# Performance work log

Measured on AMD Instinct MI355X. Metric: run time of the kernel, lower is better.

## Reference

```python
import jax, jax.numpy as jnp
import numpy as np

NC, NV, C, H, L = 60000, 256, 128, 4, 3
D = C // H
E1, E2 = 600000, 240000
VPG = 4  # virtual nodes per graph; batch = NV // VPG = 64


def setup_inputs() -> dict:
    key = jax.random.key(0)
    ks = iter(jax.random.split(key, 64))
    def rn(shape, scale=1.0):
        return jax.random.normal(next(ks), shape, dtype=jnp.float32) * scale
    sC = 1.0 / np.sqrt(C)
    sD = 1.0 / np.sqrt(D)
    return dict(
        x_cell=rn((NC, C)), x_vcell=rn((NV, C)),
        Wk=rn((L, 2, C, C), sC), bk=jnp.zeros((L, 2, C), jnp.float32),
        Wq=rn((L, 2, C, C), sC), bq=jnp.zeros((L, 2, C), jnp.float32),
        Wv=rn((L, 2, C, C), sC), bv=jnp.zeros((L, 2, C), jnp.float32),
        Wa=rn((L, 2, C, C), sC), ba=jnp.zeros((L, 2, C), jnp.float32),
        skip=jnp.ones((L, 2), jnp.float32),
        arel=rn((L, 2, H, D, D), sD), mrel=rn((L, 2, H, D, D), sD),
        prel=jnp.ones((L, 2, H), jnp.float32),
        Wk_o=rn((L, C, 1), sC), bk_o=jnp.zeros((L, 1), jnp.float32),
        Wq_o=rn((L, C, 1), sC), bq_o=jnp.zeros((L, 1), jnp.float32),
        Wv_o=rn((L, C, 1), sC), bv_o=jnp.zeros((L, 1), jnp.float32),
        Wa_o=rn((L, 1, 1)), ba_o=jnp.zeros((L, 1), jnp.float32),
        arel_o=jnp.ones((L, 1, 1, 1), jnp.float32),
        mrel_o=jnp.ones((L, 1, 1, 1), jnp.float32),
        prel_o=jnp.ones((L, 1), jnp.float32),
        fc_W=rn((VPG, 1), 0.5), fc_b=jnp.zeros((1,), jnp.float32),
        mlp_W1=rn((1, 2)), mlp_b1=jnp.zeros((2,), jnp.float32),
        mlp_W2=rn((2, 1), 0.7), mlp_b2=jnp.zeros((1,), jnp.float32),
        src_cc=jax.random.randint(next(ks), (E1,), 0, NC, dtype=jnp.int32),
        dst_cc=jax.random.randint(next(ks), (E1,), 0, NC, dtype=jnp.int32),
        src_cv=jax.random.randint(next(ks), (E2,), 0, NC, dtype=jnp.int32),
        dst_cv=jax.random.randint(next(ks), (E2,), 0, NV, dtype=jnp.int32),
    )


def _seg_softmax(logits, seg, n):
    # numerically stable softmax over edges grouped by destination node
    m = jax.ops.segment_max(logits, seg, num_segments=n)
    e = jnp.exp(logits - m[seg])
    s = jax.ops.segment_sum(e, seg, num_segments=n)
    return e / s[seg]


def _attn(k_src, q_dst, v_src, a_r, m_r, p_r, src, dst, n_dst, d):
    # HGT relation-specific attention: gather -> softmax per dst -> scatter
    krel = jnp.einsum('nhd,hde->nhe', k_src, a_r)
    vrel = jnp.einsum('nhd,hde->nhe', v_src, m_r)
    logits = (q_dst[dst] * krel[src]).sum(-1) * p_r / jnp.sqrt(jnp.float32(d))  # [E,H]
    alpha = _seg_softmax(logits, dst, n_dst)
    return jax.ops.segment_sum(alpha[..., None] * vrel[src], dst, num_segments=n_dst)


def _forward(x_cell, x_vcell, Wk, bk, Wq, bq, Wv, bv, Wa, ba, skip,
             arel, mrel, prel, Wk_o, bk_o, Wq_o, bq_o, Wv_o, bv_o, Wa_o, ba_o,
             arel_o, mrel_o, prel_o, fc_W, fc_b, mlp_W1, mlp_b1, mlp_W2, mlp_b2,
             src_cc, dst_cc, src_cv, dst_cv):
    nc, nv = x_cell.shape[0], x_vcell.shape[0]
    gelu = jax.nn.gelu
    xc, xv = x_cell, x_vcell
    outs = []
    for li in range(L):
        def lin(x, W, b):
            return (x @ W + b).reshape(x.shape[0], H, D)
        kc = lin(xc, Wk[li, 0], bk[li, 0])
        qc = lin(xc, Wq[li, 0], bq[li, 0])
        vc = lin(xc, Wv[li, 0], bv[li, 0])
        qv = lin(xv, Wq[li, 1], bq[li, 1])
        # in_conv: cell->cell and cell->vcell message passing
        agg_c = _attn(kc, qc, vc, arel[li, 0], mrel[li, 0], prel[li, 0], src_cc, dst_cc, nc, D)
        agg_v = _attn(kc, qv, vc, arel[li, 1], mrel[li, 1], prel[li, 1], src_cv, dst_cv, nv, D)
        oc = gelu(agg_c.reshape(nc, C)) @ Wa[li, 0] + ba[li, 0]
        ov = gelu(agg_v.reshape(nv, C)) @ Wa[li, 1] + ba[li, 1]
        bc = jax.nn.sigmoid(skip[li, 0])
        bvv = jax.nn.sigmoid(skip[li, 1])
        xc = bc * oc + (1.0 - bc) * xc
        xv = bvv * ov + (1.0 - bvv) * xv
        # out_conv (hid->1, 1 head) on virtual edges only
        ko = (xc @ Wk_o[li] + bk_o[li]).reshape(nc, 1, 1)
        qo = (xv @ Wq_o[li] + bq_o[li]).reshape(nv, 1, 1)
        vo = (xc @ Wv_o[li] + bv_o[li]).reshape(nc, 1, 1)
        aggo = _attn(ko, qo, vo, arel_o[li], mrel_o[li], prel_o[li], src_cv, dst_cv, nv, 1)
        outs.append(gelu(aggo.reshape(nv, 1)) @ Wa_o[li] + ba_o[li])
    jk = jnp.max(jnp.stack(outs, axis=-1), axis=-1)  # JK 'max' over layers -> [NV,1]
    h = jk.reshape(-1, fc_W.shape[0])                # [B, VPG]
    h = gelu(h @ fc_W + fc_b)                        # node_fc
    h = gelu(h @ mlp_W1 + mlp_b1)                    # MLP hidden (dropout=0)
    out = h @ mlp_W2 + mlp_b2
    return out.squeeze(1)                            # [B]


def reference(x_cell, x_vcell, Wk, bk, Wq, bq, Wv, bv, Wa, ba, skip,
              arel, mrel, prel, Wk_o, bk_o, Wq_o, bq_o, Wv_o, bv_o, Wa_o, ba_o,
              arel_o, mrel_o, prel_o, fc_W, fc_b, mlp_W1, mlp_b1, mlp_W2, mlp_b2,
              src_cc, dst_cc, src_cv, dst_cv):
    return _forward(x_cell, x_vcell, Wk, bk, Wq, bq, Wv, bv, Wa, ba, skip,
                    arel, mrel, prel, Wk_o, bk_o, Wq_o, bq_o, Wv_o, bv_o, Wa_o, ba_o,
                    arel_o, mrel_o, prel_o, fc_W, fc_b, mlp_W1, mlp_b1, mlp_W2, mlp_b2,
                    src_cc, dst_cc, src_cv, dst_cv)
```

## Files before the change

kernel.cpp:

```cpp
#include <hip/hip_runtime.h>
#include <hip/hip_fp16.h>
#include <math.h>
#include <stdint.h>

#define N_C 60000
#define N_V 256
#define CH 128
#define NH 4
#define HD 32
#define NL 3
#define NE1 600000
#define NE2 240000

#define CDIV(a,b) (((a)+(b)-1)/(b))
#define EPB 1024


typedef _Float16 f16x8 __attribute__((ext_vector_type(8)));
typedef _Float16 f16x4 __attribute__((ext_vector_type(4)));
typedef float f32x4 __attribute__((ext_vector_type(4)));
typedef float f32x2 __attribute__((ext_vector_type(2)));

__device__ __forceinline__ float gelu_tanh(float x) {
    float x3 = x * x * x;
// ... 55 lines not shown
__global__ __launch_bounds__(128) void cvt_w16(
    const float* __restrict__ WQT, const float* __restrict__ Wk,
    const float* __restrict__ WVT, const float* __restrict__ Wa,
    _Float16* __restrict__ WT16)
{
    int b = blockIdx.x;
    int li = b / 5, w = b % 5;
    const float* src;
    if      (w == 0) src = WQT + (size_t)(li * 2) * CH * CH;
    else if (w == 1) src = Wk  + (size_t)(li * 2) * CH * CH;
    else if (w == 2) src = WVT + (size_t)(li * 2) * CH * CH;
    else if (w == 3) src = WVT + (size_t)(li * 2 + 1) * CH * CH;
    else             src = Wa  + (size_t)(li * 2) * CH * CH;
    _Float16* dst = WT16 + (size_t)b * CH * CH;
    for (int o = threadIdx.x; o < CH * CH; o += 128) {
        int i = o & 7, lane = (o >> 3) & 63, f = (o >> 9) & 7, kk = o >> 12;
        int mr = lane & 15, g = lane >> 4;
        int k = kk * 32 + g * 8 + i;
        int c = (w < 4) ? (mr * 8 + f) : (f * 16 + mr);
        dst[o] = (_Float16)src[k * CH + c];
    }
}

__global__ __launch_bounds__(256) void bucket_hist(const int* __restrict__ dst, int E,
                                                   int shift, int* __restrict__ bhist)
{
    __shared__ int h[256];
    int t = threadIdx.x;
    h[t] = 0;
    __syncthreads();
    int i0 = blockIdx.x * EPB, i1 = min(i0 + EPB, E);
    for (int i = i0 + t; i < i1; i += 256)
        atomicAdd(&h[(dst[i] >> shift) & 255], 1);
    __syncthreads();
    if (h[t] > 0) atomicAdd(&bhist[t], h[t]);
}

__global__ __launch_bounds__(256) void scan256(const int* __restrict__ h,
                                               int* __restrict__ base, int* __restrict__ cur)
{
    __shared__ int p[256];
    int t = threadIdx.x;
    int v = h[t];
    p[t] = v;
    __syncthreads();
    for (int off = 1; off < 256; off <<= 1) {
        int u = (t >= off) ? p[t - off] : 0;
        __syncthreads();
        p[t] += u;
        __syncthreads();
    }
    base[t] = p[t] - v;
    cur[t]  = p[t] - v;
    if (t == 255) base[256] = p[255];
}

template<bool PAIR>
__global__ __launch_bounds__(256) void partition_edges(
    const int* __restrict__ src, const int* __restrict__ dst, int E, int shift,
    int* __restrict__ cur, int2* __restrict__ tmp_pair, int* __restrict__ out_src)
{
    __shared__ int cnt[256], base[256], cnt2[256];
    int t = threadIdx.x;
    cnt[t] = 0; cnt2[t] = 0;
    __syncthreads();
    int i0 = blockIdx.x * EPB, i1 = min(i0 + EPB, E);
    for (int i = i0 + t; i < i1; i += 256)
        atomicAdd(&cnt[(dst[i] >> shift) & 255], 1);
    __syncthreads();
    if (cnt[t] > 0) base[t] = atomicAdd(&cur[t], cnt[t]);
    __syncthreads();
    for (int i = i0 + t; i < i1; i += 256) {
        int d = dst[i];
        int dig = (d >> shift) & 255;
        int r = atomicAdd(&cnt2[dig], 1);
        int pos = base[dig] + r;
        if constexpr (PAIR) tmp_pair[pos] = make_int2(src[i], d);
        else                out_src[pos] = src[i];
    }
}

__global__ __launch_bounds__(256) void bucket_finalize(
    const int2* __restrict__ tmp, const int* __restrict__ bbase, int n, int NE,
    int* __restrict__ rs, int* __restrict__ csr)
{
    __shared__ int cnt[256], pre[256], cnt2[256];
    int b = blockIdx.x, t = threadIdx.x;
    int s0 = bbase[b], s1 = bbase[b + 1];
    cnt[t] = 0; cnt2[t] = 0;
    __syncthreads();
    for (int i = s0 + t; i < s1; i += 256)
        atomicAdd(&cnt[tmp[i].y & 255], 1);
    __syncthreads();
    int v = cnt[t];
    pre[t] = v;
    __syncthreads();
    for (int off = 1; off < 256; off <<= 1) {
        int u = (t >= off) ? pre[t - off] : 0;
        __syncthreads();
        pre[t] += u;
        __syncthreads();
    }
    pre[t] -= v;
    __syncthreads();
    int dstid = b * 256 + t;
    if (dstid < n) rs[dstid] = s0 + pre[t];
    if (b == 0 && t == 0) rs[n] = NE;
    for (int i = s0 + t; i < s1; i += 256) {
        int2 e = tmp[i];
        int low = e.y & 255;
        int r = atomicAdd(&cnt2[low], 1);
        csr[s0 + pre[low] + r] = e.x;
    }
}

__global__ __launch_bounds__(256) void gemm_qkv(
    int nblk1,
    const float* __restrict__ A, int lda, int M,
    const _Float16* __restrict__ WT4,
    const float* __restrict__ b0, const float* __restrict__ b1,
    const float* __restrict__ b2, const float* __restrict__ b3,
    float* __restrict__ out, unsigned char* __restrict__ kv8,
    const float* __restrict__ qo, const float* __restrict__ ko, const float* __restrict__ vo,
    const int* __restrict__ rs_cv, const int* __restrict__ csr_cv,
    const float* __restrict__ arel_o, const float* __restrict__ prel_o,
    const float* __restrict__ mrel_o, const float* __restrict__ Wa_o,
    const float* __restrict__ ba_o, float* __restrict__ outl)
{
    extern __shared__ char dynsm[];
    __shared__ float sms[4], sma[4];
    int tid = threadIdx.x;

    if ((int)blockIdx.x >= nblk1) {
        int node = blockIdx.x - nblk1;
        float qs = qo[node] * arel_o[0] * prel_o[0];
        int rs = rs_cv[node], re = rs_cv[node + 1];
        float s = 0.f, a = 0.f;
        for (int e = rs + tid; e < re; e += 256) {
            int si = csr_cv[e];
            float w = __expf(qs * ko[si]);
            s += w;
            a = fmaf(w, vo[si], a);
        }
        #pragma unroll
        for (int off = 32; off >= 1; off >>= 1) {
            s += __shfl_xor(s, off, 64);
            a += __shfl_xor(a, off, 64);
        }
        int lane = tid & 63, wid = tid >> 6;
        if (lane == 0) { sms[wid] = s; sma[wid] = a; }
        __syncthreads();
        if (tid == 0) {
            float S = sms[0] + sms[1] + sms[2] + sms[3];
            float A_ = sma[0] + sma[1] + sma[2] + sma[3];
            float agg = (S > 0.f) ? A_ / S : 0.f;
            agg *= mrel_o[0];
            outl[node] = gelu_tanh(agg) * Wa_o[0] + ba_o[0];
        }
        return;
    }

    _Float16 (*Af)[136] = (_Float16(*)[136])dynsm;
    int row0 = blockIdx.x * 64;
    #pragma unroll
    for (int i = 0; i < 8; i++) {
        int slot = tid + i * 256;
        int r = slot >> 5, q = slot & 31;
        int rr = row0 + r;
        float4 v = make_float4(0.f, 0.f, 0.f, 0.f);
        if (rr < M) v = *(const float4*)(A + (size_t)rr * lda + q * 4);
        f16x4 h = { (_Float16)v.x, (_Float16)v.y, (_Float16)v.z, (_Float16)v.w };
        *(f16x4*)&Af[r][q * 4] = h;
    }
    __syncthreads();

    int lane = tid & 63, w = tid >> 6;
    int mr = lane & 15, g = lane >> 4;
    f16x8 afr[4];
    #pragma unroll
    for (int kk = 0; kk < 4; kk++)
        afr[kk] = *(const f16x8*)&Af[w * 16 + mr][kk * 32 + g * 8];
    __syncthreads();

// ... 46 lines not shown
                float v2 = acc[2][r] + bias[2], v3 = acc[3][r] + bias[3];
                float v4 = acc[4][r] + bias[4], v5 = acc[5][r] + bias[5];
                float v6 = acc[6][r] + bias[6], v7 = acc[7][r] + bias[7];
                unsigned int lo = (unsigned)__builtin_amdgcn_cvt_pk_fp8_f32(v0, v1, 0, false);
                lo = (unsigned)__builtin_amdgcn_cvt_pk_fp8_f32(v2, v3, (int)lo, true);
                unsigned int hi = (unsigned)__builtin_amdgcn_cvt_pk_fp8_f32(v4, v5, 0, false);
                hi = (unsigned)__builtin_amdgcn_cvt_pk_fp8_f32(v6, v7, (int)hi, true);
                if (jw == 1) {
                    kp[r] = make_uint2(lo, hi);
                } else {
                    int row = row0 + w * 16 + g * 4 + r;
                    if (row < M) {
                        unsigned char* base = kv8 + ((size_t)row << 9) + mr * 16
                                            + ((jw == 3) ? 256 : 0);
                        *(uint4*)base = make_uint4(kp[r].x, kp[r].y, lo, hi);
                    }
                }
            }
        }
        __syncthreads();
    }
}

__global__ __launch_bounds__(256) void gemm128(
    int nblk1,
    const float* __restrict__ A1, int lda1, const _Float16* __restrict__ W1h,
    const float* __restrict__ bias1, float* __restrict__ out1, int M1,
    const float* __restrict__ gate1, const float* __restrict__ xold1,
    const float* __restrict__ wk1, const float* __restrict__ bk1, float* __restrict__ ko1,
    const float* __restrict__ wv1, const float* __restrict__ bv1, float* __restrict__ vo1,
    const float* __restrict__ A2, int lda2, const float* __restrict__ W2,
    const float* __restrict__ bias2, float* __restrict__ out2, int M2,
    const float* __restrict__ gate2, const float* __restrict__ xold2,
    const float* __restrict__ wk2, const float* __restrict__ bk2, float* __restrict__ ko2)
{
    extern __shared__ char dynsm[];
    int tid = threadIdx.x;

    if ((int)blockIdx.x < nblk1) {
        _Float16 (*Af)[136] = (_Float16(*)[136])dynsm;
        int row0 = blockIdx.x * 64;
        #pragma unroll
        for (int i = 0; i < 8; i++) {
            int slot = tid + i * 256;
            int r = slot >> 5, q = slot & 31;
            int rr = row0 + r;
            float4 v = make_float4(0.f, 0.f, 0.f, 0.f);
            if (rr < M1) v = *(const float4*)(A1 + (size_t)rr * lda1 + q * 4);
            f16x4 h = { (_Float16)v.x, (_Float16)v.y, (_Float16)v.z, (_Float16)v.w };
            *(f16x4*)&Af[r][q * 4] = h;
        }
        __syncthreads();

        int lane = tid & 63, w = tid >> 6;
        int mr = lane & 15, g = lane >> 4;
        f16x8 afr[4];
        #pragma unroll
        for (int kk = 0; kk < 4; kk++)
            afr[kk] = *(const f16x8*)&Af[w * 16 + mr][kk * 32 + g * 8];
        __syncthreads();

        _Float16* Bl = (_Float16*)dynsm;
        uint4* Blv = (uint4*)dynsm;
        const uint4* WTv = (const uint4*)W1h;
        uint4 tmp[8];
        #pragma unroll
        for (int i = 0; i < 8; i++) tmp[i] = WTv[tid + i * 256];
        #pragma unroll
        for (int i = 0; i < 8; i++) Blv[tid + i * 256] = tmp[i];
        __syncthreads();

        f32x4 acc[8] = {};
        #pragma unroll
        for (int kk = 0; kk < 4; kk++) {
            f16x8 bf[8];
            #pragma unroll
            for (int f = 0; f < 8; f++)
                bf[f] = *(const f16x8*)(Bl + (size_t)((kk * 8 + f) * 64 + lane) * 8);
            #pragma unroll
            for (int f = 0; f < 8; f++)
                acc[f] = __builtin_amdgcn_mfma_f32_16x16x32_f16(afr[kk], bf[f], acc[f], 0, 0, 0);
        }

        float gt = 1.f / (1.f + expf(-gate1[0]));
        float og = 1.f - gt;
        float pk[4] = {}, pv[4] = {};
        #pragma unroll
        for (int f = 0; f < 8; f++) {
            int col = f * 16 + mr;
            float bias = bias1[col];
            float wkc = wk1[col];
            float wvc = wv1[col];
            #pragma unroll
            for (int r = 0; r < 4; r++) {
                int row = row0 + w * 16 + g * 4 + r;
                if (row < M1) {
                    float v = acc[f][r] + bias;
                    v = gt * v + og * xold1[(size_t)row * 128 + col];
                    out1[(size_t)row * 128 + col] = v;
                    pk[r] = fmaf(v, wkc, pk[r]);
                    pv[r] = fmaf(v, wvc, pv[r]);
                }
            }
        }
        #pragma unroll
        for (int r = 0; r < 4; r++) {
            #pragma unroll
            for (int off = 1; off < 16; off <<= 1) {
                pk[r] += __shfl_xor(pk[r], off, 64);
                pv[r] += __shfl_xor(pv[r], off, 64);
            }
        }
        if (mr == 0) {
            #pragma unroll
            for (int r = 0; r < 4; r++) {
                int row = row0 + w * 16 + g * 4 + r;
                if (row < M1) {
                    ko1[row] = pk[r] + bk1[0];
                    vo1[row] = pv[r] + bv1[0];
                }
            }
        }
        return;
    }

    float (*As)[36]  = (float(*)[36])dynsm;
    float (*Bs)[128] = (float(*)[128])(dynsm + 64 * 36 * 4);
    const float* A    = A2;
    int lda           = lda2;
    const float* W    = W2;
    const float* bias = bias2;
    float* out        = out2;
    int M             = M2;
    const float* gate = gate2;
    const float* xold = xold2;
    const float* wk_o = wk2;
    const float* bk_o = bk2;
    float* ko         = ko2;

    int row0 = (blockIdx.x - nblk1) * 64;
    int tx = tid & 15;
    int ty = tid >> 4;
    float acc[4][8] = {};
    for (int k0 = 0; k0 < 128; k0 += 32) {
        __syncthreads();
        #pragma unroll
        for (int i = 0; i < 2; i++) {
            int slot = tid + i * 256;
            int r = slot >> 3, kq = slot & 7;
            int rr = row0 + r;
            float4 v = make_float4(0.f, 0.f, 0.f, 0.f);
            if (rr < M) v = *(const float4*)(A + (size_t)rr * lda + k0 + kq * 4);
            *(float4*)&As[r][kq * 4] = v;
        }
        #pragma unroll
        for (int i = 0; i < 4; i++) {
            int slot = tid + i * 256;
            int kr = slot >> 5, cq = slot & 31;
            *(float4*)&Bs[kr][cq * 4] = *(const float4*)(W + (size_t)(k0 + kr) * 128 + cq * 4);
        }
        __syncthreads();
        #pragma unroll
        for (int k4 = 0; k4 < 32; k4 += 4) {
            float4 av[4];
            #pragma unroll
            for (int i = 0; i < 4; i++)
                av[i] = *(const float4*)&As[ty * 4 + i][k4];
            #pragma unroll
            for (int kk = 0; kk < 4; kk++) {
                float4 bl = *(const float4*)&Bs[k4 + kk][tx * 4];
                float4 bh = *(const float4*)&Bs[k4 + kk][64 + tx * 4];
                float bb[8] = {bl.x, bl.y, bl.z, bl.w, bh.x, bh.y, bh.z, bh.w};
                #pragma unroll
                for (int i = 0; i < 4; i++) {
                    float a = ((const float*)&av[i])[kk];
                    #pragma unroll
                    for (int j = 0; j < 8; j++)
                        acc[i][j] = fmaf(a, bb[j], acc[i][j]);
                }
            }
        }
    }
    float gt = 1.f / (1.f + expf(-gate[0]));
    float og = 1.f - gt;
    float wkr[8];
    #pragma unroll
    for (int j = 0; j < 4; j++) {
        wkr[j]     = wk_o[tx * 4 + j];
        wkr[4 + j] = wk_o[64 + tx * 4 + j];
    }
    #pragma unroll
    for (int i = 0; i < 4; i++) {
        int r = row0 + ty * 4 + i;
        if (r >= M) continue;
        float vals[8];
        #pragma unroll
        for (int j = 0; j < 4; j++) {
            float v0 = acc[i][j]     + bias[tx * 4 + j];
            float v1 = acc[i][4 + j] + bias[64 + tx * 4 + j];
            v0 = gt * v0 + og * xold[(size_t)r * 128 + tx * 4 + j];
            v1 = gt * v1 + og * xold[(size_t)r * 128 + 64 + tx * 4 + j];
            vals[j] = v0;
            vals[4 + j] = v1;
        }
        float* op = out + (size_t)r * 128;
        *(float4*)(op + tx * 4)      = make_float4(vals[0], vals[1], vals[2], vals[3]);
        *(float4*)(op + 64 + tx * 4) = make_float4(vals[4], vals[5], vals[6], vals[7]);
        float pk = 0.f;
        #pragma unroll
        for (int j = 0; j < 8; j++) pk = fmaf(vals[j], wkr[j], pk);
        #pragma unroll
        for (int off = 1; off < 16; off <<= 1)
            pk += __shfl_xor(pk, off, 64);
        if (tx == 0) ko[r] = pk + bk_o[0];
    }
}

__device__ __forceinline__ void gather_cv(
    const unsigned char* __restrict__ kv8, const int* __restrict__ csr,
    int e0, int e1, int g, int j, const float* q8,
    float& s_io, float acc[8])
{
    int lane = threadIdx.x & 63;
    float s = s_io;
    for (int cs = e0; cs < e1; cs += 64) {
        int n = e1 - cs; if (n > 64) n = 64;
        int nm1 = n - 1;
        int idx0 = 0;
        if (lane < n) idx0 = csr[cs + lane];
        int R = (n + 7) >> 3;
        uint4 a0, a1, b0, b1;

#define LD2(E0_, E1_, B0_, B1_) { \
            int i0_ = __shfl(idx0, min((E0_), nm1), 64); \
            int i1_ = __shfl(idx0, min((E1_), nm1), 64); \
            B0_ = *(const uint4*)(kv8 + ((size_t)i0_ << 9) + 256 + (j << 4)); \
            B1_ = *(const uint4*)(kv8 + ((size_t)i1_ << 9) + 256 + (j << 4)); }
// ... 24 lines not shown
        if (R > 1) LD2(g + 8, g + 12, b0, b1);
        for (int r = 0; r < R; r += 2) {
            int er = g + 8 * r;
            CMP2(er, er + 4, a0, a1);
            if (r + 2 < R) LD2(g + 8 * (r + 2), g + 8 * (r + 2) + 4, a0, a1);
            if (r + 1 < R) {
                int eo = g + 8 * (r + 1);
                CMP2(eo, eo + 4, b0, b1);
                if (r + 3 < R) LD2(g + 8 * (r + 3), g + 8 * (r + 3) + 4, b0, b1);
            }
        }
#undef LD2
#undef CMP2
    }
    s_io = s;
}

__global__ __launch_bounds__(256) void attn_uni(
    float* __restrict__ xq, const unsigned char* __restrict__ kv8,
    const float* __restrict__ xv, const float* __restrict__ wqt,
    const float* __restrict__ bqt,
    const int* __restrict__ rs_cc, const int* __restrict__ csr_cc,
    const int* __restrict__ rs_cv, const int* __restrict__ csr_cv,
    float* __restrict__ aggv, int n_c)
{
    __shared__ float smem[656];
    int lane = threadIdx.x & 63, wid = threadIdx.x >> 6;
    int g = lane >> 4, j = lane & 15;

    if (blockIdx.x < N_V) {
        int node = blockIdx.x;
        float* qrow = smem;
        float* sm_s = smem + 128;
        float* sm_a = smem + 144;
        if (wid < 2) {
            int col = wid * 64 + lane;
            float a = bqt[col];
            const float* xr = xv + (size_t)node * 128;
            for (int k = 0; k < 128; k++)
                a = fmaf(xr[k], wqt[(size_t)k * 128 + col], a);
            qrow[col] = a;
        }
        __syncthreads();
        float q8[8];
        *(float4*)&q8[0] = *(const float4*)&qrow[8 * j];
        *(float4*)&q8[4] = *(const float4*)&qrow[8 * j + 4];
        int rs = rs_cv[node], re = rs_cv[node + 1];
// ... 11 lines not shown
        s += __shfl_xor(s, 16, 64);
        s += __shfl_xor(s, 32, 64);
        if (g == 0) {
            *(float4*)&sm_a[wid * 128 + 8 * j]     = make_float4(acc[0], acc[1], acc[2], acc[3]);
            *(float4*)&sm_a[wid * 128 + 8 * j + 4] = make_float4(acc[4], acc[5], acc[6], acc[7]);
            if ((j & 3) == 0) sm_s[wid * 4 + (j >> 2)] = s;
        }
        __syncthreads();
        if (threadIdx.x < 64) {
            int lp = 2 * lane;
            int h = lp >> 5;
            float S = 0.f, AX = 0.f, AY = 0.f;
            #pragma unroll
            for (int i = 0; i < 4; i++) {
                S  += sm_s[i * 4 + h];
                float2 a2 = *(const float2*)&sm_a[i * 128 + lp];
                AX += a2.x;
                AY += a2.y;
            }
            float inv = (S > 0.f) ? 1.f / S : 0.f;
            aggv[(size_t)node * 128 + lp]     = gelu_tanh(AX * inv);
            aggv[(size_t)node * 128 + lp + 1] = gelu_tanh(AY * inv);
        }
    } else {
        int node = (blockIdx.x - N_V) * 16 + wid * 4 + g;
        bool valid = (node < n_c);
        int rs = valid ? rs_cc[node] : 0;
        int re = valid ? rs_cc[node + 1] : 0;
        float q8[8];
        if (valid) {
            const float* qp = xq + (size_t)node * 128 + 8 * j;
            *(float4*)&q8[0] = *(const float4*)qp;
            *(float4*)&q8[4] = *(const float4*)(qp + 4);
        } else {
            #pragma unroll
            for (int i = 0; i < 8; i++) q8[i] = 0.f;
        }
        float s = 0.f;
        float acc[8] = {};
        int base = lane & 48;

        for (int cs = rs; cs < re; cs += 16) {
            int cnt = min(16, re - cs);
            int cm1 = cnt - 1;
            int idx = csr_cc[cs + min(j, cm1)];
            uint4 B0, B1, B2, B3;

// ... 27 lines not shown
                if (cnt > 10) { LDE(10, B2) LDE(11, B3) }
                if (cnt > 8) {
                    CMPE(8, B0) CMPE(9, B1)
                    if (cnt > 12) { LDE(12, B0) LDE(13, B1) }
                    CMPE(10, B2) CMPE(11, B3)
                    if (cnt > 14) { LDE(14, B2) LDE(15, B3) }
                    if (cnt > 12) {
                        CMPE(12, B0) CMPE(13, B1) CMPE(14, B2) CMPE(15, B3)
                    }
                }
            }
#undef LDE
#undef CMPE
        }
        if (valid) {
            float inv = (s > 0.f) ? 1.f / s : 0.f;
            float4 o0 = make_float4(gelu_tanh(acc[0] * inv), gelu_tanh(acc[1] * inv),
                                    gelu_tanh(acc[2] * inv), gelu_tanh(acc[3] * inv));
            float4 o1 = make_float4(gelu_tanh(acc[4] * inv), gelu_tanh(acc[5] * inv),
                                    gelu_tanh(acc[6] * inv), gelu_tanh(acc[7] * inv));
            float* op = xq + (size_t)node * 128 + 8 * j;
            *(float4*)op = o0;
            *(float4*)(op + 4) = o1;
        }
    }
}

__global__ __launch_bounds__(256) void attn_out(
    const float* __restrict__ qo, const float* __restrict__ ko, const float* __restrict__ vo,
    const int* __restrict__ rowstart, const int* __restrict__ csr,
    const float* __restrict__ arel_o, const float* __restrict__ prel_o,
    const float* __restrict__ mrel_o, const float* __restrict__ Wa_o,
    const float* __restrict__ ba_o, float* __restrict__ outl)
{
    int node = blockIdx.x;
    float qs = qo[node] * arel_o[0] * prel_o[0];
    int rs = rowstart[node], re = rowstart[node + 1];
    float s = 0.f, a = 0.f;
    for (int e = rs + (int)threadIdx.x; e < re; e += 256) {
        int si = csr[e];
        float w = __expf(qs * ko[si]);
        s += w;
        a = fmaf(w, vo[si], a);
    }
    #pragma unroll
    for (int off = 32; off >= 1; off >>= 1) {
// ... 91 lines not shown
    unsigned char* KV8 = (unsigned char*)alloc((size_t)N_C * 512);
    float* AGGV = (float*)alloc(sizeof(float) * (size_t)N_V * CH);
    float* KO   = (float*)alloc(sizeof(float) * N_C);
    float* VO   = (float*)alloc(sizeof(float) * N_C);
    float* QO   = (float*)alloc(sizeof(float) * N_V);
    float* OUTS = (float*)alloc(sizeof(float) * NL * N_V);
    int* bhist    = (int*)alloc(sizeof(int) * 512);
    int* bhist_cc = bhist;
    int* bhist_cv = bhist + 256;
    int* bbase_cc = (int*)alloc(sizeof(int) * 257);
    int* cur_cc   = (int*)alloc(sizeof(int) * 256);
    int* cur_cv   = (int*)alloc(sizeof(int) * 256);
    int* rs_cc    = (int*)alloc(sizeof(int) * (N_C + 1));
    int* rs_cv    = (int*)alloc(sizeof(int) * (N_V + 1));
    int* csr_cc   = (int*)alloc(sizeof(int) * NE1);
    int* csr_cv   = (int*)alloc(sizeof(int) * NE2);
    int2* tmp_cc  = (int2*)alloc(sizeof(int2) * NE1);

    const int tot_c = NL * 2 * (CH + 1) * CH;
    compose_w<true ><<<CDIV(tot_c, 256), 256, 0, stream>>>(Wq, bq, arel, prel, WQT, BQT);
    compose_w<false><<<CDIV(tot_c, 256), 256, 0, stream>>>(Wv, bv, mrel, nullptr, WVT, BVT);
    cvt_w16<<<NL * 5, 128, 0, stream>>>(WQT, Wk, WVT, Wa, WT16);
    hipMemsetAsync(bhist, 0, sizeof(int) * 512, stream);
    bucket_hist<<<CDIV(NE1, EPB), 256, 0, stream>>>(dst_cc, NE1, 8, bhist_cc);
    bucket_hist<<<CDIV(NE2, EPB), 256, 0, stream>>>(dst_cv, NE2, 0, bhist_cv);
    scan256<<<1, 256, 0, stream>>>(bhist_cc, bbase_cc, cur_cc);
    scan256<<<1, 256, 0, stream>>>(bhist_cv, rs_cv, cur_cv);
    partition_edges<true ><<<CDIV(NE1, EPB), 256, 0, stream>>>(src_cc, dst_cc, NE1, 8,
                                                               cur_cc, tmp_cc, nullptr);
    partition_edges<false><<<CDIV(NE2, EPB), 256, 0, stream>>>(src_cv, dst_cv, NE2, 0,
                                                               cur_cv, nullptr, csr_cv);
    bucket_finalize<<<CDIV(N_C, 256), 256, 0, stream>>>(tmp_cc, bbase_cc, N_C, NE1,
                                                        rs_cc, csr_cc);

    const int gb_c = CDIV(N_C, 64);
    const int gb_v = CDIV(N_V, 64);
    const int gb_attn = N_V + CDIV(N_C, 16);
    const int SM_QKV = 32768;
    const int SM_128 = 32768;

    for (int li = 0; li < NL; li++) {
        const float* xc_src = (li == 0) ? x_cell : XC;
        const float* xv_src = (li == 0) ? x_vcell : XV;
        size_t w1 = (size_t)(li * 2 + 1) * CH * CH;
        int b0 = (li * 2) * CH, b1 = (li * 2 + 1) * CH;
        const _Float16* WT5 = WT16 + (size_t)(li * 5) * CH * CH;
        const _Float16* WT_a = WT16 + (size_t)(li * 5 + 4) * CH * CH;

        int tail = (li > 0) ? N_V : 0;
        gemm_qkv<<<gb_c + tail, 256, SM_QKV, stream>>>(
            gb_c, xc_src, 128, N_C,
            WT5,
            BQT + b0, bk + b0, BVT + b0, BVT + b1, XQ, KV8,
            QO, KO, VO, rs_cv, csr_cv,
            arel_o + (li - 1), prel_o + (li - 1), mrel_o + (li - 1),
            Wa_o + (li - 1), ba_o + (li - 1),
            (li > 0) ? (OUTS + (li - 1) * N_V) : nullptr);

        attn_uni<<<gb_attn, 256, 0, stream>>>(
            XQ, KV8, xv_src, WQT + w1, BQT + b1,
            rs_cc, csr_cc, rs_cv, csr_cv,
            AGGV, N_C);

        gemm128<<<gb_c + gb_v, 256, SM_128, stream>>>(
            gb_c,
            XQ, 128, WT_a, ba + b0, XC, N_C,
            skip + li * 2, xc_src,
            Wk_o + li * CH, bk_o + li, KO,
            Wv_o + li * CH, bv_o + li, VO,
            AGGV, 128, Wa + w1, ba + b1, XV, N_V,
            skip + li * 2 + 1, xv_src,
            Wq_o + li * CH, bq_o + li, QO);
    }

    attn_out<<<N_V, 256, 0, stream>>>(QO, KO, VO, rs_cv, csr_cv,
                                      arel_o + (NL - 1), prel_o + (NL - 1), mrel_o + (NL - 1),
                                      Wa_o + (NL - 1), ba_o + (NL - 1), OUTS + (NL - 1) * N_V);
    final_head<<<1, 64, 0, stream>>>(OUTS, fc_W, fc_b, mlp_W1, mlp_b1, mlp_W2, mlp_b2,
                                     (float*)d_out);
}
```

Before: 535.2 us.

## Fuse next-layer QKV GEMM into output GEMM epilogue and merge preprocessing launches

New measurement: 507.0 us. -5.3%, faster.

```diff
diff --git a/kernel.cpp b/kernel.cpp
--- a/kernel.cpp
+++ b/kernel.cpp
@@ -101,24 +101,36 @@
     }
 }
 
-__global__ __launch_bounds__(256) void bucket_hist(const int* __restrict__ dst, int E,
-                                                   int shift, int* __restrict__ bhist)
+__global__ __launch_bounds__(256) void bucket_hist2(
+    const int* __restrict__ dcc, const int* __restrict__ dcv, int nb_cc,
+    int* __restrict__ hcc, int* __restrict__ hcv)
 {
     __shared__ int h[256];
+    bool cv = (int)blockIdx.x >= nb_cc;
+    const int* dst = cv ? dcv : dcc;
+    int E = cv ? NE2 : NE1;
+    int shift = cv ? 0 : 8;
+    int* bh = cv ? hcv : hcc;
+    int b = cv ? blockIdx.x - nb_cc : blockIdx.x;
     int t = threadIdx.x;
     h[t] = 0;
     __syncthreads();
-    int i0 = blockIdx.x * EPB, i1 = min(i0 + EPB, E);
+    int i0 = b * EPB, i1 = min(i0 + EPB, E);
     for (int i = i0 + t; i < i1; i += 256)
         atomicAdd(&h[(dst[i] >> shift) & 255], 1);
     __syncthreads();
-    if (h[t] > 0) atomicAdd(&bhist[t], h[t]);
-}
-
-__global__ __launch_bounds__(256) void scan256(const int* __restrict__ h,
-                                               int* __restrict__ base, int* __restrict__ cur)
+    if (h[t] > 0) atomicAdd(&bh[t], h[t]);
+}
+
+__global__ __launch_bounds__(256) void scan256x2(
+    const int* __restrict__ hcc, int* __restrict__ base_cc, int* __restrict__ cur_cc,
+    const int* __restrict__ hcv, int* __restrict__ base_cv, int* __restrict__ cur_cv)
 {
     __shared__ int p[256];
+    bool cv = blockIdx.x > 0;
+    const int* h  = cv ? hcv : hcc;
+    int* base     = cv ? base_cv : base_cc;
+    int* cur      = cv ? cur_cv : cur_cc;
     int t = threadIdx.x;
     int v = h[t];
     p[t] = v;
@@ -134,16 +146,24 @@
     if (t == 255) base[256] = p[255];
 }
 
-template<bool PAIR>
-__global__ __launch_bounds__(256) void partition_edges(
-    const int* __restrict__ src, const int* __restrict__ dst, int E, int shift,
-    int* __restrict__ cur, int2* __restrict__ tmp_pair, int* __restrict__ out_src)
+__global__ __launch_bounds__(256) void partition2(
+    const int* __restrict__ scc, const int* __restrict__ dcc,
+    const int* __restrict__ scv, const int* __restrict__ dcv, int nb_cc,
+    int* __restrict__ cur_cc, int* __restrict__ cur_cv,
+    int2* __restrict__ tmp_pair, int* __restrict__ out_src)
 {
     __shared__ int cnt[256], base[256], cnt2[256];
+    bool cv = (int)blockIdx.x >= nb_cc;
+    const int* src = cv ? scv : scc;
+    const int* dst = cv ? dcv : dcc;
+    int E = cv ? NE2 : NE1;
+    int shift = cv ? 0 : 8;
+    int* cur = cv ? cur_cv : cur_cc;
+    int b = cv ? blockIdx.x - nb_cc : blockIdx.x;
     int t = threadIdx.x;
     cnt[t] = 0; cnt2[t] = 0;
     __syncthreads();
-    int i0 = blockIdx.x * EPB, i1 = min(i0 + EPB, E);
+    int i0 = b * EPB, i1 = min(i0 + EPB, E);
     for (int i = i0 + t; i < i1; i += 256)
         atomicAdd(&cnt[(dst[i] >> shift) & 255], 1);
     __syncthreads();
@@ -154,8 +174,8 @@
         int dig = (d >> shift) & 255;
         int r = atomicAdd(&cnt2[dig], 1);
         int pos = base[dig] + r;
-        if constexpr (PAIR) tmp_pair[pos] = make_int2(src[i], d);
-        else                out_src[pos] = src[i];
+        if (cv) out_src[pos] = src[i];
+        else    tmp_pair[pos] = make_int2(src[i], d);
     }
 }
 
@@ -194,50 +214,14 @@
 }
 
 __global__ __launch_bounds__(256) void gemm_qkv(
-    int nblk1,
     const float* __restrict__ A, int lda, int M,
     const _Float16* __restrict__ WT4,
     const float* __restrict__ b0, const float* __restrict__ b1,
     const float* __restrict__ b2, const float* __restrict__ b3,
-    float* __restrict__ out, unsigned char* __restrict__ kv8,
-    const float* __restrict__ qo, const float* __restrict__ ko, const float* __restrict__ vo,
-    const int* __restrict__ rs_cv, const int* __restrict__ csr_cv,
-    const float* __restrict__ arel_o, const float* __restrict__ prel_o,
-    const float* __restrict__ mrel_o, const float* __restrict__ Wa_o,
-    const float* __restrict__ ba_o, float* __restrict__ outl)
+    float* __restrict__ out, unsigned char* __restrict__ kv8)
 {
     extern __shared__ char dynsm[];
-    __shared__ float sms[4], sma[4];
     int tid = threadIdx.x;
-
-    if ((int)blockIdx.x >= nblk1) {
-        int node = blockIdx.x - nblk1;
-        float qs = qo[node] * arel_o[0] * prel_o[0];
-        int rs = rs_cv[node], re = rs_cv[node + 1];
-        float s = 0.f, a = 0.f;
-        for (int e = rs + tid; e < re; e += 256) {
-            int si = csr_cv[e];
-            float w = __expf(qs * ko[si]);
-            s += w;
-            a = fmaf(w, vo[si], a);
-        }
-        #pragma unroll
-        for (int off = 32; off >= 1; off >>= 1) {
-            s += __shfl_xor(s, off, 64);
-            a += __shfl_xor(a, off, 64);
-        }
-        int lane = tid & 63, wid = tid >> 6;
-        if (lane == 0) { sms[wid] = s; sma[wid] = a; }
-        __syncthreads();
-        if (tid == 0) {
-            float S = sms[0] + sms[1] + sms[2] + sms[3];
-            float A_ = sma[0] + sma[1] + sma[2] + sma[3];
-            float agg = (S > 0.f) ? A_ / S : 0.f;
-            agg *= mrel_o[0];
-            outl[node] = gelu_tanh(agg) * Wa_o[0] + ba_o[0];
-        }
-        return;
-    }
 
     _Float16 (*Af)[136] = (_Float16(*)[136])dynsm;
     int row0 = blockIdx.x * 64;
@@ -330,13 +314,17 @@
     }
 }
 
-__global__ __launch_bounds__(256) void gemm128(
-    int nblk1,
-    const float* __restrict__ A1, int lda1, const _Float16* __restrict__ W1h,
-    const float* __restrict__ bias1, float* __restrict__ out1, int M1,
+__global__ __launch_bounds__(256) void gemm_fused(
+    int nblk1, int do_qkv,
+    const float* __restrict__ A1, const _Float16* __restrict__ Wa_h,
+    const float* __restrict__ bias1, float* __restrict__ xc_out, int M,
     const float* __restrict__ gate1, const float* __restrict__ xold1,
     const float* __restrict__ wk1, const float* __restrict__ bk1, float* __restrict__ ko1,
     const float* __restrict__ wv1, const float* __restrict__ bv1, float* __restrict__ vo1,
+    const _Float16* __restrict__ WT4,
+    const float* __restrict__ qb0, const float* __restrict__ qb1,
+    const float* __restrict__ qb2, const float* __restrict__ qb3,
+    float* __restrict__ xq_out, unsigned char* __restrict__ kv8,
     const float* __restrict__ A2, int lda2, const float* __restrict__ W2,
     const float* __restrict__ bias2, float* __restrict__ out2, int M2,
     const float* __restrict__ gate2, const float* __restrict__ xold2,
@@ -345,32 +333,198 @@
     extern __shared__ char dynsm[];
     int tid = threadIdx.x;
 
-    if ((int)blockIdx.x < nblk1) {
-        _Float16 (*Af)[136] = (_Float16(*)[136])dynsm;
-        int row0 = blockIdx.x * 64;
-        #pragma unroll
-        for (int i = 0; i < 8; i++) {
-            int slot = tid + i * 256;
-            int r = slot >> 5, q = slot & 31;
-            int rr = row0 + r;
-            float4 v = make_float4(0.f, 0.f, 0.f, 0.f);
-            if (rr < M1) v = *(const float4*)(A1 + (size_t)rr * lda1 + q * 4);
-            f16x4 h = { (_Float16)v.x, (_Float16)v.y, (_Float16)v.z, (_Float16)v.w };
-            *(f16x4*)&Af[r][q * 4] = h;
-        }
-        __syncthreads();
-
-        int lane = tid & 63, w = tid >> 6;
-        int mr = lane & 15, g = lane >> 4;
-        f16x8 afr[4];
-        #pragma unroll
-        for (int kk = 0; kk < 4; kk++)
-            afr[kk] = *(const f16x8*)&Af[w * 16 + mr][kk * 32 + g * 8];
-        __syncthreads();
-
-        _Float16* Bl = (_Float16*)dynsm;
-        uint4* Blv = (uint4*)dynsm;
-        const uint4* WTv = (const uint4*)W1h;
+    if ((int)blockIdx.x >= nblk1) {
+        float (*As)[36]  = (float(*)[36])dynsm;
+        float (*Bs)[128] = (float(*)[128])(dynsm + 64 * 36 * 4);
+        int row0 = (blockIdx.x - nblk1) * 64;
+        int tx = tid & 15;
+        int ty = tid >> 4;
+        float acc[4][8] = {};
+        for (int k0 = 0; k0 < 128; k0 += 32) {
+            __syncthreads();
+            #pragma unroll
+            for (int i = 0; i < 2; i++) {
+                int slot = tid + i * 256;
+                int r = slot >> 3, kq = slot & 7;
+                int rr = row0 + r;
+                float4 v = make_float4(0.f, 0.f, 0.f, 0.f);
+                if (rr < M2) v = *(const float4*)(A2 + (size_t)rr * lda2 + k0 + kq * 4);
+                *(float4*)&As[r][kq * 4] = v;
+            }
+            #pragma unroll
+            for (int i = 0; i < 4; i++) {
+                int slot = tid + i * 256;
+                int kr = slot >> 5, cq = slot & 31;
+                *(float4*)&Bs[kr][cq * 4] = *(const float4*)(W2 + (size_t)(k0 + kr) * 128 + cq * 4);
+            }
+            __syncthreads();
+            #pragma unroll
+            for (int k4 = 0; k4 < 32; k4 += 4) {
+                float4 av[4];
+                #pragma unroll
+                for (int i = 0; i < 4; i++)
+                    av[i] = *(const float4*)&As[ty * 4 + i][k4];
+                #pragma unroll
+                for (int kk = 0; kk < 4; kk++) {
+                    float4 bl = *(const float4*)&Bs[k4 + kk][tx * 4];
+                    float4 bh = *(const float4*)&Bs[k4 + kk][64 + tx * 4];
+                    float bb[8] = {bl.x, bl.y, bl.z, bl.w, bh.x, bh.y, bh.z, bh.w};
+                    #pragma unroll
+                    for (int i = 0; i < 4; i++) {
+                        float a = ((const float*)&av[i])[kk];
+                        #pragma unroll
+                        for (int j = 0; j < 8; j++)
+                            acc[i][j] = fmaf(a, bb[j], acc[i][j]);
+                    }
+                }
+            }
+        }
+        float gt = 1.f / (1.f + expf(-gate2[0]));
+        float og = 1.f - gt;
+        float wkr[8];
+        #pragma unroll
+        for (int j = 0; j < 4; j++) {
+            wkr[j]     = wk2[tx * 4 + j];
+            wkr[4 + j] = wk2[64 + tx * 4 + j];
+        }
+        #pragma unroll
+        for (int i = 0; i < 4; i++) {
+            int r = row0 + ty * 4 + i;
+            if (r >= M2) continue;
+            float vals[8];
+            #pragma unroll
+            for (int j = 0; j < 4; j++) {
+                float v0 = acc[i][j]     + bias2[tx * 4 + j];
+                float v1 = acc[i][4 + j] + bias2[64 + tx * 4 + j];
+                v0 = gt * v0 + og * xold2[(size_t)r * 128 + tx * 4 + j];
+                v1 = gt * v1 + og * xold2[(size_t)r * 128 + 64 + tx * 4 + j];
+                vals[j] = v0;
+                vals[4 + j] = v1;
+            }
+            float* op = out2 + (size_t)r * 128;
+            *(float4*)(op + tx * 4)      = make_float4(vals[0], vals[1], vals[2], vals[3]);
+            *(float4*)(op + 64 + tx * 4) = make_float4(vals[4], vals[5], vals[6], vals[7]);
+            float pk = 0.f;
+            #pragma unroll
+            for (int j = 0; j < 8; j++) pk = fmaf(vals[j], wkr[j], pk);
+            #pragma unroll
+            for (int off = 1; off < 16; off <<= 1)
+                pk += __shfl_xor(pk, off, 64);
+            if (tx == 0) ko2[r] = pk + bk2[0];
+        }
+        return;
+    }
+
+    _Float16 (*Af)[136] = (_Float16(*)[136])dynsm;
+    int row0 = blockIdx.x * 64;
+    #pragma unroll
+    for (int i = 0; i < 8; i++) {
+        int slot = tid + i * 256;
+        int r = slot >> 5, q = slot & 31;
+        int rr = row0 + r;
+        float4 v = make_float4(0.f, 0.f, 0.f, 0.f);
+        if (rr < M) v = *(const float4*)(A1 + (size_t)rr * 128 + q * 4);
+        f16x4 h = { (_Float16)v.x, (_Float16)v.y, (_Float16)v.z, (_Float16)v.w };
+        *(f16x4*)&Af[r][q * 4] = h;
+    }
+    __syncthreads();
+
+    int lane = tid & 63, w = tid >> 6;
+    int mr = lane & 15, g = lane >> 4;
+    f16x8 afr[4];
+    #pragma unroll
+    for (int kk = 0; kk < 4; kk++)
+        afr[kk] = *(const f16x8*)&Af[w * 16 + mr][kk * 32 + g * 8];
+    __syncthreads();
+
+    _Float16* Bl = (_Float16*)dynsm;
+    uint4* Blv = (uint4*)dynsm;
+    {
+        const uint4* WTv = (const uint4*)Wa_h;
+        uint4 tmp[8];
+        #pragma unroll
+        for (int i = 0; i < 8; i++) tmp[i] = WTv[tid + i * 256];
+        #pragma unroll
+        for (int i = 0; i < 8; i++) Blv[tid + i * 256] = tmp[i];
+    }
+    __syncthreads();
+
+    f32x4 acc[8] = {};
+    #pragma unroll
+    for (int kk = 0; kk < 4; kk++) {
+        f16x8 bf[8];
+        #pragma unroll
+        for (int f = 0; f < 8; f++)
+            bf[f] = *(const f16x8*)(Bl + (size_t)((kk * 8 + f) * 64 + lane) * 8);
+        #pragma unroll
+        for (int f = 0; f < 8; f++)
+            acc[f] = __builtin_amdgcn_mfma_f32_16x16x32_f16(afr[kk], bf[f], acc[f], 0, 0, 0);
+    }
+    __syncthreads();
+
+    float gt = 1.f / (1.f + expf(-gate1[0]));
+    float og = 1.f - gt;
+    float vals[8][4];
+    float pk[4] = {}, pv[4] = {};
+    #pragma unroll
+    for (int f = 0; f < 8; f++) {
+        int col = f * 16 + mr;
+        float bias = bias1[col];
+        float wkc = wk1[col];
+        float wvc = wv1[col];
+        #pragma unroll
+        for (int r = 0; r < 4; r++) {
+            int row = row0 + w * 16 + g * 4 + r;
+            float v = 0.f;
+            if (row < M) {
+                v = acc[f][r] + bias;
+                v = gt * v + og * xold1[(size_t)row * 128 + col];
+                xc_out[(size_t)row * 128 + col] = v;
+                pk[r] = fmaf(v, wkc, pk[r]);
+                pv[r] = fmaf(v, wvc, pv[r]);
+            }
+            vals[f][r] = v;
+        }
+    }
+    #pragma unroll
+    for (int r = 0; r < 4; r++) {
+        #pragma unroll
+        for (int off = 1; off < 16; off <<= 1) {
+            pk[r] += __shfl_xor(pk[r], off, 64);
+            pv[r] += __shfl_xor(pv[r], off, 64);
+        }
+    }
+    if (mr == 0) {
+        #pragma unroll
+        for (int r = 0; r < 4; r++) {
+            int row = row0 + w * 16 + g * 4 + r;
+            if (row < M) {
+                ko1[row] = pk[r] + bk1[0];
+                vo1[row] = pv[r] + bv1[0];
+            }
+        }
+    }
+
+    if (!do_qkv) return;
+
+    #pragma unroll
+    for (int f = 0; f < 8; f++) {
+        int col = f * 16 + mr;
+        #pragma unroll
+        for (int r = 0; r < 4; r++)
+            Af[w * 16 + g * 4 + r][col] = (_Float16)vals[f][r];
+    }
+    __syncthreads();
+    f16x8 afr2[4];
+    #pragma unroll
+    for (int kk = 0; kk < 4; kk++)
+        afr2[kk] = *(const f16x8*)&Af[w * 16 + mr][kk * 32 + g * 8];
+    __syncthreads();
+
+    const float* bs[4] = {qb0, qb1, qb2, qb3};
+    uint2 kp[4];
+    for (int jw = 0; jw < 4; jw++) {
+        const uint4* WTv = (const uint4*)(WT4 + (size_t)jw * CH * CH);
         uint4 tmp[8];
         #pragma unroll
         for (int i = 0; i < 8; i++) tmp[i] = WTv[tid + i * 256];
@@ -378,7 +532,7 @@
         for (int i = 0; i < 8; i++) Blv[tid + i * 256] = tmp[i];
         __syncthreads();
 
-        f32x4 acc[8] = {};
+        f32x4 acc2[8] = {};
         #pragma unroll
         for (int kk = 0; kk < 4; kk++) {
             f16x8 bf[8];
@@ -387,140 +541,50 @@
                 bf[f] = *(const f16x8*)(Bl + (size_t)((kk * 8 + f) * 64 + lane) * 8);
             #pragma unroll
             for (int f = 0; f < 8; f++)
-                acc[f] = __builtin_amdgcn_mfma_f32_16x16x32_f16(afr[kk], bf[f], acc[f], 0, 0, 0);
-        }
-
-        float gt = 1.f / (1.f + expf(-gate1[0]));
-        float og = 1.f - gt;
-        float pk[4] = {}, pv[4] = {};
-        #pragma unroll
-        for (int f = 0; f < 8; f++) {
-            int col = f * 16 + mr;
-            float bias = bias1[col];
-            float wkc = wk1[col];
-            float wvc = wv1[col];
+                acc2[f] = __builtin_amdgcn_mfma_f32_16x16x32_f16(afr2[kk], bf[f], acc2[f], 0, 0, 0);
+        }
+        const float* bb = bs[jw];
+        float4 blo = *(const float4*)&bb[mr * 8];
+        float4 bhi = *(const float4*)&bb[mr * 8 + 4];
+        float bias[8] = {blo.x, blo.y, blo.z, blo.w, bhi.x, bhi.y, bhi.z, bhi.w};
+        if (jw == 0) {
             #pragma unroll
             for (int r = 0; r < 4; r++) {
                 int row = row0 + w * 16 + g * 4 + r;
-                if (row < M1) {
-                    float v = acc[f][r] + bias;
-                    v = gt * v + og * xold1[(size_t)row * 128 + col];
-                    out1[(size_t)row * 128 + col] = v;
-                    pk[r] = fmaf(v, wkc, pk[r]);
-                    pv[r] = fmaf(v, wvc, pv[r]);
+                if (row < M) {
+                    float4 o0 = make_float4(acc2[0][r] + bias[0], acc2[1][r] + bias[1],
+                                            acc2[2][r] + bias[2], acc2[3][r] + bias[3]);
+                    float4 o1 = make_float4(acc2[4][r] + bias[4], acc2[5][r] + bias[5],
+                                            acc2[6][r] + bias[6], acc2[7][r] + bias[7]);
+                    float* op = xq_out + (size_t)row * 128 + mr * 8;
+                    *(float4*)op = o0;
+                    *(float4*)(op + 4) = o1;
                 }
             }
-        }
-        #pragma unroll
-        for (int r = 0; r < 4; r++) {
-            #pragma unroll
-            for (int off = 1; off < 16; off <<= 1) {
-                pk[r] += __shfl_xor(pk[r], off, 64);
-                pv[r] += __shfl_xor(pv[r], off, 64);
-            }
-        }
-        if (mr == 0) {
+        } else {
             #pragma unroll
             for (int r = 0; r < 4; r++) {
-                int row = row0 + w * 16 + g * 4 + r;
-                if (row < M1) {
-                    ko1[row] = pk[r] + bk1[0];
-                    vo1[row] = pv[r] + bv1[0];
+                float v0 = acc2[0][r] + bias[0], v1 = acc2[1][r] + bias[1];
+                float v2 = acc2[2][r] + bias[2], v3 = acc2[3][r] + bias[3];
+                float v4 = acc2[4][r] + bias[4], v5 = acc2[5][r] + bias[5];
+                float v6 = acc2[6][r] + bias[6], v7 = acc2[7][r] + bias[7];
+                unsigned int lo = (unsigned)__builtin_amdgcn_cvt_pk_fp8_f32(v0, v1, 0, false);
+                lo = (unsigned)__builtin_amdgcn_cvt_pk_fp8_f32(v2, v3, (int)lo, true);
+                unsigned int hi = (unsigned)__builtin_amdgcn_cvt_pk_fp8_f32(v4, v5, 0, false);
+                hi = (unsigned)__builtin_amdgcn_cvt_pk_fp8_f32(v6, v7, (int)hi, true);
+                if (jw == 1) {
+                    kp[r] = make_uint2(lo, hi);
+                } else {
+                    int row = row0 + w * 16 + g * 4 + r;
+                    if (row < M) {
+                        unsigned char* base = kv8 + ((size_t)row << 9) + mr * 16
+                                            + ((jw == 3) ? 256 : 0);
+                        *(uint4*)base = make_uint4(kp[r].x, kp[r].y, lo, hi);
+                    }
                 }
             }
         }
-        return;
-    }
-
-    float (*As)[36]  = (float(*)[36])dynsm;
-    float (*Bs)[128] = (float(*)[128])(dynsm + 64 * 36 * 4);
-    const float* A    = A2;
-    int lda           = lda2;
-    const float* W    = W2;
-    const float* bias = bias2;
-    float* out        = out2;
-    int M             = M2;
-    const float* gate = gate2;
-    const float* xold = xold2;
-    const float* wk_o = wk2;
-    const float* bk_o = bk2;
-    float* ko         = ko2;
-
-    int row0 = (blockIdx.x - nblk1) * 64;
-    int tx = tid & 15;
-    int ty = tid >> 4;
-    float acc[4][8] = {};
-    for (int k0 = 0; k0 < 128; k0 += 32) {
         __syncthreads();
-        #pragma unroll
-        for (int i = 0; i < 2; i++) {
-            int slot = tid + i * 256;
-            int r = slot >> 3, kq = slot & 7;
-            int rr = row0 + r;
-            float4 v = make_float4(0.f, 0.f, 0.f, 0.f);
-            if (rr < M) v = *(const float4*)(A + (size_t)rr * lda + k0 + kq * 4);
-            *(float4*)&As[r][kq * 4] = v;
-        }
-        #pragma unroll
-        for (int i = 0; i < 4; i++) {
-            int slot = tid + i * 256;
-            int kr = slot >> 5, cq = slot & 31;
-            *(float4*)&Bs[kr][cq * 4] = *(const float4*)(W + (size_t)(k0 + kr) * 128 + cq * 4);
-        }
-        __syncthreads();
-        #pragma unroll
-        for (int k4 = 0; k4 < 32; k4 += 4) {
-            float4 av[4];
-            #pragma unroll
-            for (int i = 0; i < 4; i++)
-                av[i] = *(const float4*)&As[ty * 4 + i][k4];
-            #pragma unroll
-            for (int kk = 0; kk < 4; kk++) {
-                float4 bl = *(const float4*)&Bs[k4 + kk][tx * 4];
-                float4 bh = *(const float4*)&Bs[k4 + kk][64 + tx * 4];
-                float bb[8] = {bl.x, bl.y, bl.z, bl.w, bh.x, bh.y, bh.z, bh.w};
-                #pragma unroll
-                for (int i = 0; i < 4; i++) {
-                    float a = ((const float*)&av[i])[kk];
-                    #pragma unroll
-                    for (int j = 0; j < 8; j++)
-                        acc[i][j] = fmaf(a, bb[j], acc[i][j]);
-                }
-            }
-        }
-    }
-    float gt = 1.f / (1.f + expf(-gate[0]));
-    float og = 1.f - gt;
-    float wkr[8];
-    #pragma unroll
-    for (int j = 0; j < 4; j++) {
-        wkr[j]     = wk_o[tx * 4 + j];
-        wkr[4 + j] = wk_o[64 + tx * 4 + j];
-    }
-    #pragma unroll
-    for (int i = 0; i < 4; i++) {
-        int r = row0 + ty * 4 + i;
-        if (r >= M) continue;
-        float vals[8];
-        #pragma unroll
-        for (int j = 0; j < 4; j++) {
-            float v0 = acc[i][j]     + bias[tx * 4 + j];
-            float v1 = acc[i][4 + j] + bias[64 + tx * 4 + j];
-            v0 = gt * v0 + og * xold[(size_t)r * 128 + tx * 4 + j];
-            v1 = gt * v1 + og * xold[(size_t)r * 128 + 64 + tx * 4 + j];
-            vals[j] = v0;
-            vals[4 + j] = v1;
-        }
-        float* op = out + (size_t)r * 128;
-        *(float4*)(op + tx * 4)      = make_float4(vals[0], vals[1], vals[2], vals[3]);
-        *(float4*)(op + 64 + tx * 4) = make_float4(vals[4], vals[5], vals[6], vals[7]);
-        float pk = 0.f;
-        #pragma unroll
-        for (int j = 0; j < 8; j++) pk = fmaf(vals[j], wkr[j], pk);
-        #pragma unroll
-        for (int off = 1; off < 16; off <<= 1)
-            pk += __shfl_xor(pk, off, 64);
-        if (tx == 0) ko[r] = pk + bk_o[0];
     }
 }
 
@@ -591,7 +655,12 @@
     const float* __restrict__ bqt,
     const int* __restrict__ rs_cc, const int* __restrict__ csr_cc,
     const int* __restrict__ rs_cv, const int* __restrict__ csr_cv,
-    float* __restrict__ aggv, int n_c)
+    float* __restrict__ aggv, int n_c, int ccb,
+    const float* __restrict__ qo, const float* __restrict__ ko,
+    const float* __restrict__ vo,
+    const float* __restrict__ arel_o, const float* __restrict__ prel_o,
+    const float* __restrict__ mrel_o, const float* __restrict__ Wa_o,
+    const float* __restrict__ ba_o, float* __restrict__ outl)
 {
     __shared__ float smem[656];
     int lane = threadIdx.x & 63, wid = threadIdx.x >> 6;
@@ -649,7 +718,7 @@
             aggv[(size_t)node * 128 + lp]     = gelu_tanh(AX * inv);
             aggv[(size_t)node * 128 + lp + 1] = gelu_tanh(AY * inv);
         }
-    } else {
+    } else if ((int)blockIdx.x < N_V + ccb) {
         int node = (blockIdx.x - N_V) * 16 + wid * 4 + g;
         bool valid = (node < n_c);
         int rs = valid ? rs_cc[node] : 0;
@@ -723,6 +792,33 @@
             float* op = xq + (size_t)node * 128 + 8 * j;
             *(float4*)op = o0;
             *(float4*)(op + 4) = o1;
+        }
+    } else {
+        int node = blockIdx.x - N_V - ccb;
+        float* sms = smem;
+        float* sma = smem + 4;
+        float qs = qo[node] * arel_o[0] * prel_o[0];
+        int rs = rs_cv[node], re = rs_cv[node + 1];
+        float s = 0.f, a = 0.f;
+        for (int e = rs + (int)threadIdx.x; e < re; e += 256) {
+            int si = csr_cv[e];
+            float w = __expf(qs * ko[si]);
+            s += w;
+            a = fmaf(w, vo[si], a);
+        }
+        #pragma unroll
+        for (int off = 32; off >= 1; off >>= 1) {
+            s += __shfl_xor(s, off, 64);
+            a += __shfl_xor(a, off, 64);
+        }
+        if (lane == 0) { sms[wid] = s; sma[wid] = a; }
+        __syncthreads();
+        if (threadIdx.x == 0) {
+            float S = sms[0] + sms[1] + sms[2] + sms[3];
+            float A = sma[0] + sma[1] + sma[2] + sma[3];
+            float agg = (S > 0.f) ? A / S : 0.f;
+            agg *= mrel_o[0];
+            outl[node] = gelu_tanh(agg) * Wa_o[0] + ba_o[0];
         }
     }
 }
@@ -860,55 +956,59 @@
     compose_w<false><<<CDIV(tot_c, 256), 256, 0, stream>>>(Wv, bv, mrel, nullptr, WVT, BVT);
     cvt_w16<<<NL * 5, 128, 0, stream>>>(WQT, Wk, WVT, Wa, WT16);
     hipMemsetAsync(bhist, 0, sizeof(int) * 512, stream);
-    bucket_hist<<<CDIV(NE1, EPB), 256, 0, stream>>>(dst_cc, NE1, 8, bhist_cc);
-    bucket_hist<<<CDIV(NE2, EPB), 256, 0, stream>>>(dst_cv, NE2, 0, bhist_cv);
-    scan256<<<1, 256, 0, stream>>>(bhist_cc, bbase_cc, cur_cc);
-    scan256<<<1, 256, 0, stream>>>(bhist_cv, rs_cv, cur_cv);
-    partition_edges<true ><<<CDIV(NE1, EPB), 256, 0, stream>>>(src_cc, dst_cc, NE1, 8,
-                                                               cur_cc, tmp_cc, nullptr);
-    partition_edges<false><<<CDIV(NE2, EPB), 256, 0, stream>>>(src_cv, dst_cv, NE2, 0,
-                                                               cur_cv, nullptr, csr_cv);
+    const int nb_cc = CDIV(NE1, EPB), nb_cv = CDIV(NE2, EPB);
+    bucket_hist2<<<nb_cc + nb_cv, 256, 0, stream>>>(dst_cc, dst_cv, nb_cc,
+                                                    bhist_cc, bhist_cv);
+    scan256x2<<<2, 256, 0, stream>>>(bhist_cc, bbase_cc, cur_cc,
+                                     bhist_cv, rs_cv, cur_cv);
+    partition2<<<nb_cc + nb_cv, 256, 0, stream>>>(src_cc, dst_cc, src_cv, dst_cv, nb_cc,
+                                                  cur_cc, cur_cv, tmp_cc, csr_cv);
     bucket_finalize<<<CDIV(N_C, 256), 256, 0, stream>>>(tmp_cc, bbase_cc, N_C, NE1,
                                                         rs_cc, csr_cc);
 
     const int gb_c = CDIV(N_C, 64);
     const int gb_v = CDIV(N_V, 64);
-    const int gb_attn = N_V + CDIV(N_C, 16);
-    const int SM_QKV = 32768;
-    const int SM_128 = 32768;
+    const int ccb = CDIV(N_C, 16);
+    const int SM_BIG = 32768;
+
+    gemm_qkv<<<gb_c, 256, SM_BIG, stream>>>(
+        x_cell, 128, N_C,
+        WT16, BQT, bk, BVT, BVT + CH, XQ, KV8);
+    attn_uni<<<N_V + ccb, 256, 0, stream>>>(
+        XQ, KV8, x_vcell, WQT + (size_t)CH * CH, BQT + CH,
+        rs_cc, csr_cc, rs_cv, csr_cv, AGGV, N_C, ccb,
+        nullptr, nullptr, nullptr, nullptr, nullptr, nullptr, nullptr, nullptr, nullptr);
 
     for (int li = 0; li < NL; li++) {
         const float* xc_src = (li == 0) ? x_cell : XC;
         const float* xv_src = (li == 0) ? x_vcell : XV;
+        int b0 = (li * 2) * CH, b1 = (li * 2 + 1) * CH;
         size_t w1 = (size_t)(li * 2 + 1) * CH * CH;
-        int b0 = (li * 2) * CH, b1 = (li * 2 + 1) * CH;
-        const _Float16* WT5 = WT16 + (size_t)(li * 5) * CH * CH;
         const _Float16* WT_a = WT16 + (size_t)(li * 5 + 4) * CH * CH;
-
-        int tail = (li > 0) ? N_V : 0;
-        gemm_qkv<<<gb_c + tail, 256, SM_QKV, stream>>>(
-            gb_c, xc_src, 128, N_C,
-            WT5,
-            BQT + b0, bk + b0, BVT + b0, BVT + b1, XQ, KV8,
-            QO, KO, VO, rs_cv, csr_cv,
-            arel_o + (li - 1), prel_o + (li - 1), mrel_o + (li - 1),
-            Wa_o + (li - 1), ba_o + (li - 1),
-            (li > 0) ? (OUTS + (li - 1) * N_V) : nullptr);
-
-        attn_uni<<<gb_attn, 256, 0, stream>>>(
-            XQ, KV8, xv_src, WQT + w1, BQT + b1,
-            rs_cc, csr_cc, rs_cv, csr_cv,
-            AGGV, N_C);
-
-        gemm128<<<gb_c + gb_v, 256, SM_128, stream>>>(
-            gb_c,
-            XQ, 128, WT_a, ba + b0, XC, N_C,
+        int do_qkv = (li + 1 < NL) ? 1 : 0;
+        const _Float16* WT5n = WT16 + (size_t)((li + 1) % NL * 5) * CH * CH;
+        int nb0 = ((li + 1) % NL * 2) * CH, nb1 = ((li + 1) % NL * 2 + 1) * CH;
+
+        gemm_fused<<<gb_c + gb_v, 256, SM_BIG, stream>>>(
+            gb_c, do_qkv,
+            XQ, WT_a, ba + b0, XC, N_C,
             skip + li * 2, xc_src,
             Wk_o + li * CH, bk_o + li, KO,
             Wv_o + li * CH, bv_o + li, VO,
+            WT5n, BQT + nb0, bk + nb0, BVT + nb0, BVT + nb1, XQ, KV8,
             AGGV, 128, Wa + w1, ba + b1, XV, N_V,
             skip + li * 2 + 1, xv_src,
             Wq_o + li * CH, bq_o + li, QO);
+
+        if (do_qkv) {
+            size_t w1n = (size_t)((li + 1) * 2 + 1) * CH * CH;
+            attn_uni<<<N_V + ccb + N_V, 256, 0, stream>>>(
+                XQ, KV8, XV, WQT + w1n, BQT + (li + 1) * 2 * CH + CH,
+                rs_cc, csr_cc, rs_cv, csr_cv, AGGV, N_C, ccb,
+                QO, KO, VO,
+                arel_o + li, prel_o + li, mrel_o + li,
+                Wa_o + li, ba_o + li, OUTS + li * N_V);
+        }
     }
 
     attn_out<<<N_V, 256, 0, stream>>>(QO, KO, VO, rs_cv, csr_cv,
```
